# Optimization experiments

Hardware: AMD Instinct MI355X
Metric: run time of the kernel (lower is better)

The kernel has to match this reference:

```python
import jax, jax.numpy as jnp
import numpy as np

D_MODEL = 1024
NHEAD = 16
HEAD_DIM = D_MODEL // NHEAD
D_FF = 4096
BIAS_HID = 8
EPS = 1e-5


def _pair_bias(m, w1, b1, w2, b2):
    # m: [B,S,S] -> bias [B,S,S,nhead] via per-scalar MLP 1->hid->nhead
    h = jax.nn.relu(m[..., None] * w1 + b1)          # [B,S,S,hid]
    return jnp.einsum('bxyh,hn->bxyn', h, w2) + b2   # [B,S,S,nhead]


def _layernorm(x, g, b):
    mu = jnp.mean(x, axis=-1, keepdims=True)
    var = jnp.mean(jnp.square(x - mu), axis=-1, keepdims=True)
    return (x - mu) * jax.lax.rsqrt(var + EPS) * g + b


def setup_inputs() -> dict:
    key = jax.random.key(0)
    ks = jax.random.split(key, 20)
    B, S = 4, 1024
    sc = 1.0 / np.sqrt(D_MODEL)
    inp = {
        'src': jax.random.normal(ks[0], (B, S, D_MODEL), jnp.float32),
        't_deltas': jax.random.uniform(ks[1], (B, S, S), jnp.float32),
        'dists': jax.random.uniform(ks[2], (B, S, S), jnp.float32),
        'Wq': jax.random.normal(ks[3], (D_MODEL, D_MODEL), jnp.float32) * sc,
        'bq': jnp.zeros((D_MODEL,), jnp.float32),
        'Wk': jax.random.normal(ks[4], (D_MODEL, D_MODEL), jnp.float32) * sc,
        'bk': jnp.zeros((D_MODEL,), jnp.float32),
        'Wv': jax.random.normal(ks[5], (D_MODEL, D_MODEL), jnp.float32) * sc,
        'bv': jnp.zeros((D_MODEL,), jnp.float32),
        'tb_w1': jax.random.normal(ks[6], (BIAS_HID,), jnp.float32),
        'tb_b1': jnp.zeros((BIAS_HID,), jnp.float32),
        'tb_w2': jax.random.normal(ks[7], (BIAS_HID, NHEAD), jnp.float32) * 0.3,
        'tb_b2': jnp.zeros((NHEAD,), jnp.float32),
        'db_w1': jax.random.normal(ks[8], (BIAS_HID,), jnp.float32),
        'db_b1': jnp.zeros((BIAS_HID,), jnp.float32),
        'db_w2': jax.random.normal(ks[9], (BIAS_HID, NHEAD), jnp.float32) * 0.3,
        'db_b2': jnp.zeros((NHEAD,), jnp.float32),
        'W1': jax.random.normal(ks[10], (D_MODEL, D_FF), jnp.float32) * sc,
        'b1': jnp.zeros((D_FF,), jnp.float32),
        'W2': jax.random.normal(ks[11], (D_FF, D_MODEL), jnp.float32) / np.sqrt(D_FF),
        'b2': jnp.zeros((D_MODEL,), jnp.float32),
        'g1': jnp.ones((D_MODEL,), jnp.float32),
        'beta1': jnp.zeros((D_MODEL,), jnp.float32),
        'g2': jnp.ones((D_MODEL,), jnp.float32),
        'beta2': jnp.zeros((D_MODEL,), jnp.float32),
    }
    return inp


def reference(src, t_deltas, dists, Wq, bq, Wk, bk, Wv, bv,
              tb_w1, tb_b1, tb_w2, tb_b2, db_w1, db_b1, db_w2, db_b2,
              W1, b1, W2, b2, g1, beta1, g2, beta2):
    B, S, _ = src.shape
    # QKV projections -> [B, H, S, hd]
    q = (src @ Wq + bq).reshape(B, S, NHEAD, HEAD_DIM).transpose(0, 2, 1, 3)
    k = (src @ Wk + bk).reshape(B, S, NHEAD, HEAD_DIM).transpose(0, 2, 1, 3)
    v = (src @ Wv + bv).reshape(B, S, NHEAD, HEAD_DIM).transpose(0, 2, 1, 3)
    # scores scaled by sqrt(d_model) (as in the original, not head_dim)
    scores = jnp.einsum('bhqd,bhkd->bhqk', q, k) / jnp.sqrt(jnp.float32(D_MODEL))
    bias = (_pair_bias(t_deltas, tb_w1, tb_b1, tb_w2, tb_b2)
            + _pair_bias(dists, db_w1, db_b1, db_w2, db_b2))  # [B,S,S,H]
    scores = scores + bias.transpose(0, 3, 1, 2)
    attn = jax.nn.softmax(scores, axis=-1)
    out = jnp.einsum('bhqk,bhkd->bhqd', attn, v)
    out = out.transpose(0, 2, 1, 3).reshape(B, S, D_MODEL)
    x = _layernorm(src + out, g1, beta1)
    ffn = jax.nn.relu(x @ W1 + b1) @ W2 + b2
    return _layernorm(x + ffn, g2, beta2)
```

## Files before the change

kernel.cpp:

```cpp
#include <hip/hip_runtime.h>

typedef __bf16 bf16x8 __attribute__((ext_vector_type(8)));
typedef float f32x4 __attribute__((ext_vector_type(4)));
typedef unsigned short u16;

__device__ __forceinline__ u16 f2bf(float f) {
  union { float f; unsigned u; } x; x.f = f;
  unsigned r = x.u + 0x7fffu + ((x.u >> 16) & 1u);
  return (u16)(r >> 16);
}
__device__ __forceinline__ float bf2f(u16 u) {
  union { unsigned u; float f; } x; x.u = ((unsigned)u) << 16;
  return x.f;
}
__device__ __forceinline__ void gl_lds16(const void* g, void* l) {
  __builtin_amdgcn_global_load_lds(
      (const __attribute__((address_space(1))) void*)g,
      (__attribute__((address_space(3))) void*)l, 16, 0, 0);
}

__global__ __launch_bounds__(256) void cvt_kernel(const float* __restrict__ in,
                                                  u16* __restrict__ out, int n4) {
  int i = blockIdx.x * 256 + threadIdx.x;
  if (i >= n4) return;
  float4 v = ((const float4*)in)[i];
  unsigned lo = (unsigned)f2bf(v.x) | ((unsigned)f2bf(v.y) << 16);
  unsigned hi = (unsigned)f2bf(v.z) | ((unsigned)f2bf(v.w) << 16);
  uint2 u; u.x = lo; u.y = hi;
  *(uint2*)&out[(size_t)i * 4] = u;
}

__global__ __launch_bounds__(256) void tconv_kernel(const float* __restrict__ in,
                                                    u16* __restrict__ out, int R, int C) {
  __shared__ float tile[32][33];
  int c0 = blockIdx.x * 32, r0 = blockIdx.y * 32;
  int tx = threadIdx.x & 31, ty = threadIdx.x >> 5;
#pragma unroll
  for (int i = 0; i < 4; i++)
    tile[ty + i * 8][tx] = in[(size_t)(r0 + ty + i * 8) * C + c0 + tx];
  __syncthreads();
#pragma unroll
  for (int i = 0; i < 4; i++)
    out[(size_t)(c0 + ty + i * 8) * R + r0 + tx] = f2bf(tile[tx][ty + i * 8]);
}

__global__ __launch_bounds__(256) void bcat_kernel(const float* __restrict__ bq,
                                                   const float* __restrict__ bk,
                                                   const float* __restrict__ bv,
                                                   float* __restrict__ o) {
  int i = blockIdx.x * 256 + threadIdx.x;
  if (i >= 3072) return;
  o[i] = i < 1024 ? bq[i] : (i < 2048 ? bk[i - 1024] : bv[i - 2048]);
}

template <int EPI>
__global__ __launch_bounds__(512, 2) void gemm256_kernel(const u16* __restrict__ A,
                                                         const u16* __restrict__ Bt,
                                                         const float* __restrict__ bias,
                                                         void* __restrict__ out,
                                                         int M, int N, int K,
                                                         float qscale, int kslice) {
  __shared__ u16 lds[2][2][2][8192];
  int tid = threadIdx.x, w = tid >> 6, lane = tid & 63;
  int l16 = lane & 15, lhi = lane >> 4;
  int wr = w >> 2, wc = w & 3;
  int GX = gridDim.x;
  int nwg = GX * gridDim.y;
  int nlin = blockIdx.y * GX + blockIdx.x;
  int cpx = nwg >> 3;
  int sw = (nlin & 7) * cpx + (nlin >> 3);
  int m0 = (sw / GX) * 256, n0 = (sw % GX) * 256;
  int z = blockIdx.z;
  const u16* Ag = A + (size_t)m0 * K + z * kslice;
  const u16* Bg = Bt + (size_t)n0 * K + z * kslice;
  f32x4 acc[8][4] = {};
  int niter = kslice >> 7;

  int srow0 = tid >> 2;
  int sxor = ((tid & 3) ^ ((tid >> 3) & 3)) * 8;
  int rga = (lhi ^ ((l16 >> 1) & 3)) * 8;

  auto stage = [&](int buf, int op, int kh, const u16* Gt) {
#pragma unroll
    for (int ld = 0; ld < 2; ld++)
      gl_lds16(Gt + (size_t)(ld * 128 + srow0) * K + kh * 32 + sxor,
               &lds[buf][op][kh][ld * 4096 + w * 512]);
  };
  auto rdA = [&](int buf, int kh, int mq, bf16x8* af) {
#pragma unroll
    for (int j = 0; j < 4; j++)
      af[j] = *(const bf16x8*)&lds[buf][0][kh][(wr * 128 + mq * 64 + j * 16 + l16) * 32 + rga];
  };
  auto rdB = [&](int buf, int kh, bf16x8* bfr) {
#pragma unroll
    for (int nn = 0; nn < 4; nn++)
      bfr[nn] = *(const bf16x8*)&lds[buf][1][kh][(wc * 64 + nn * 16 + l16) * 32 + rga];
  };
  auto mma16 = [&](int mq, bf16x8* af, bf16x8* bfr) {
    __builtin_amdgcn_s_setprio(1);
#pragma unroll
    for (int j = 0; j < 4; j++)
#pragma unroll
      for (int nn = 0; nn < 4; nn++)
        acc[mq * 4 + j][nn] =
            __builtin_amdgcn_mfma_f32_16x16x32_bf16(af[j], bfr[nn], acc[mq * 4 + j][nn], 0, 0, 0);
    __builtin_amdgcn_s_setprio(0);
  };

#define PH_TAIL(MQ)                                          \
  __builtin_amdgcn_s_barrier();                              \
  asm volatile("s_waitcnt lgkmcnt(0)" ::: "memory");         \
  __builtin_amdgcn_sched_barrier(0);                         \
  mma16(MQ, af, bfr);                                        \
  __builtin_amdgcn_s_barrier();

  stage(0, 0, 0, Ag);       stage(0, 1, 0, Bg);
  stage(0, 0, 1, Ag);       stage(0, 1, 1, Bg);
  stage(1, 0, 0, Ag + 64);  stage(1, 1, 0, Bg + 64);
  asm volatile("s_waitcnt vmcnt(4)" ::: "memory");
  __builtin_amdgcn_s_barrier();

  for (int j = 0; j < niter; ++j) {
    const u16* A1 = Ag + (size_t)(2 * j + 1) * 64;
    const u16* B1 = Bg + (size_t)(2 * j + 1) * 64;
    const u16* A2 = Ag + (size_t)(2 * j + 2) * 64;
    const u16* B2 = Bg + (size_t)(2 * j + 2) * 64;
    bool more = (j + 1 < niter);
    bf16x8 af[4], bfr[4];
    rdA(0, 0, 0, af); rdB(0, 0, bfr);
    stage(1, 0, 1, A1);
    PH_TAIL(0)
    rdA(0, 0, 1, af);
    stage(1, 1, 1, B1);
    PH_TAIL(1)
    rdA(0, 1, 0, af); rdB(0, 1, bfr);
    if (more) stage(0, 0, 0, A2);
    PH_TAIL(0)
    rdA(0, 1, 1, af);
    if (more) {
      stage(0, 1, 0, B2);
      asm volatile("s_waitcnt vmcnt(4)" ::: "memory");
    } else {
      asm volatile("s_waitcnt vmcnt(0)" ::: "memory");
    }
    PH_TAIL(1)
    rdA(1, 0, 0, af); rdB(1, 0, bfr);
    if (more) stage(0, 0, 1, A2);
    PH_TAIL(0)
    rdA(1, 0, 1, af);
    if (more) stage(0, 1, 1, B2);
    PH_TAIL(1)
    rdA(1, 1, 0, af); rdB(1, 1, bfr);
    if (more) stage(1, 0, 0, A2 + 64);
    PH_TAIL(0)
    rdA(1, 1, 1, af);
    if (more) {
      stage(1, 1, 0, B2 + 64);
      asm volatile("s_waitcnt vmcnt(4)" ::: "memory");
    }
    PH_TAIL(1)
  }
#undef PH_TAIL

#pragma unroll
  for (int m = 0; m < 8; m++) {
    int gr = m0 + wr * 128 + (m >> 2) * 64 + (m & 3) * 16 + lhi * 4;
#pragma unroll
    for (int nn = 0; nn < 4; nn++) {
      int gc = n0 + wc * 64 + nn * 16 + l16;
      float bv;
      if (EPI == 0 || EPI == 3) bv = (z == 0 && bias) ? bias[gc] : 0.f;
      else bv = bias[gc];
      if (EPI == 2) {
        int seg = gc >> 10, c = gc & 1023, h = c >> 6, d = c & 63;
        float sc = (seg == 0) ? qscale : 1.f;
#pragma unroll
        for (int r = 0; r < 4; r++) {
          int row = gr + r;
          int b = row >> 10, s = row & 1023;
          size_t idx = ((((size_t)seg * 4 + b) * 16 + h) * 1024 + s) * 64 + d;
          ((u16*)out)[idx] = f2bf((acc[m][nn][r] + bv) * sc);
        }
      } else if (EPI == 1) {
#pragma unroll
        for (int r = 0; r < 4; r++)
          ((u16*)out)[(size_t)(gr + r) * N + gc] = f2bf(fmaxf(acc[m][nn][r] + bv, 0.f));
      } else if (EPI == 3) {
#pragma unroll
        for (int r = 0; r < 4; r++)
          ((u16*)out)[(size_t)z * M * N + (size_t)(gr + r) * N + gc] = f2bf(acc[m][nn][r] + bv);
      } else {
#pragma unroll
        for (int r = 0; r < 4; r++)
          ((float*)out)[(size_t)z * M * N + (size_t)(gr + r) * N + gc] = acc[m][nn][r] + bv;
      }
    }
  }
}

__global__ __launch_bounds__(256) void vtrans_kernel(const u16* __restrict__ v,
                                                     u16* __restrict__ vt) {
  __shared__ u16 t[64][72];
  int bh = blockIdx.y, s0 = blockIdx.x * 64;
  int tid = threadIdx.x;
  int r = tid >> 2, c = (tid & 3) * 16;
  const u16* src = v + ((size_t)bh * 1024 + s0 + r) * 64 + c;
  *(int4*)&t[r][c] = *(const int4*)src;
  *(int4*)&t[r][c + 8] = *(const int4*)(src + 8);
  __syncthreads();
  int d = tid >> 2, sc = (tid & 3) * 16;
  u16 tmp[16];
#pragma unroll
  for (int j = 0; j < 16; j++) tmp[j] = t[sc + j][d];
  u16* dst = vt + ((size_t)bh * 64 + d) * 1024 + s0 + sc;
  *(int4*)dst = *(int4*)&tmp[0];
  *(int4*)(dst + 8) = *(int4*)&tmp[8];
}

__global__ __launch_bounds__(256) void bias_kernel(
    const float* __restrict__ td, const float* __restrict__ dd,
    const float* __restrict__ tw1, const float* __restrict__ tb1,
    const float* __restrict__ tw2, const float* __restrict__ tb2,
    const float* __restrict__ dw1, const float* __restrict__ db1,
    const float* __restrict__ dw2, const float* __restrict__ db2,
    u16* __restrict__ biasout, int b0) {
  __shared__ float stw2[128], sdw2[128], sb2[16];
  __shared__ float stw1[8], stb1[8], sdw1[8], sdb1[8];
  int tid = threadIdx.x, x = blockIdx.x, bz = blockIdx.y;
  int b = b0 + bz;
  if (tid < 128) { stw2[tid] = tw2[tid]; sdw2[tid] = dw2[tid]; }
  if (tid < 16) sb2[tid] = tb2[tid] + db2[tid];
  if (tid < 8) { stw1[tid] = tw1[tid]; stb1[tid] = tb1[tid]; sdw1[tid] = dw1[tid]; sdb1[tid] = db1[tid]; }
  __syncthreads();
  float4 tv = ((const float4*)(td + ((size_t)b * 1024 + x) * 1024))[tid];
  float4 dv = ((const float4*)(dd + ((size_t)b * 1024 + x) * 1024))[tid];
  float tj[4] = {tv.x, tv.y, tv.z, tv.w};
  float dj[4] = {dv.x, dv.y, dv.z, dv.w};
  float ht[4][8], hd[4][8];
#pragma unroll
  for (int j = 0; j < 4; j++)
#pragma unroll
    for (int i = 0; i < 8; i++) {
      ht[j][i] = fmaxf(tj[j] * stw1[i] + stb1[i], 0.f);
      hd[j][i] = fmaxf(dj[j] * sdw1[i] + sdb1[i], 0.f);
    }
  u16* outb = biasout + (size_t)bz * 16 * 1024 * 1024 + (size_t)x * 1024 + tid * 4;
#pragma unroll
  for (int h = 0; h < 16; h++) {
    float a[4];
#pragma unroll
    for (int j = 0; j < 4; j++) {
      float s = sb2[h];
#pragma unroll
      for (int i = 0; i < 8; i++)
        s += ht[j][i] * stw2[i * 16 + h] + hd[j][i] * sdw2[i * 16 + h];
      a[j] = s;
    }
    unsigned lo = (unsigned)f2bf(a[0]) | ((unsigned)f2bf(a[1]) << 16);
    unsigned hi = (unsigned)f2bf(a[2]) | ((unsigned)f2bf(a[3]) << 16);
    uint2 u; u.x = lo; u.y = hi;
    *(uint2*)&outb[(size_t)h * 1024 * 1024] = u;
  }
}

#define LDA 72
__global__ __launch_bounds__(256) void attn_kernel(
    const u16* __restrict__ qg, const u16* __restrict__ kg, const u16* __restrict__ vtg,
    const u16* __restrict__ bias, float* __restrict__ attn_out, int b0) {
  __shared__ u16 Ks[64 * LDA];
  __shared__ u16 Vt[64 * LDA];
  __shared__ u16 Ps[64 * LDA];
  int tid = threadIdx.x;
  int w = tid >> 6, l = tid & 63, l16 = l & 15, lhi = l >> 4;
  int qt = blockIdx.x, h = blockIdx.y, bz = blockIdx.z;
  int b = b0 + bz;
  size_t bh = ((size_t)(b * 16 + h)) * 1024 * 64;
  const u16* biasb = bias + (size_t)bz * 16 * 1024 * 1024 + (size_t)h * 1024 * 1024;
  int qrow = qt * 64 + w * 16 + l16;
  bf16x8 qa[2];
  qa[0] = *(const bf16x8*)&qg[bh + (size_t)qrow * 64 + lhi * 8];
  qa[1] = *(const bf16x8*)&qg[bh + (size_t)qrow * 64 + 32 + lhi * 8];

  float m_run[4], l_run[4];
  f32x4 o[4] = {};
#pragma unroll
  for (int r = 0; r < 4; r++) { m_run[r] = -1e30f; l_run[r] = 0.f; }

  int kr0 = (tid * 2) >> 3, kc0 = ((tid * 2) & 7) * 8;
  int kr1 = (tid * 2 + 1) >> 3, kc1 = ((tid * 2 + 1) & 7) * 8;

  for (int kt = 0; kt < 16; kt++) {
    __syncthreads();
    *(int4*)&Ks[kr0 * LDA + kc0] = *(const int4*)&kg[bh + (size_t)(kt * 64 + kr0) * 64 + kc0];
    *(int4*)&Ks[kr1 * LDA + kc1] = *(const int4*)&kg[bh + (size_t)(kt * 64 + kr1) * 64 + kc1];
    *(int4*)&Vt[kr0 * LDA + kc0] = *(const int4*)&vtg[bh + (size_t)kr0 * 1024 + kt * 64 + kc0];
    *(int4*)&Vt[kr1 * LDA + kc1] = *(const int4*)&vtg[bh + (size_t)kr1 * 1024 + kt * 64 + kc1];
    __syncthreads();

    f32x4 s[4] = {};
    __builtin_amdgcn_s_setprio(1);
#pragma unroll
    for (int ni = 0; ni < 4; ni++)
#pragma unroll
      for (int ks = 0; ks < 2; ks++) {
        bf16x8 kb = *(const bf16x8*)&Ks[(ni * 16 + l16) * LDA + ks * 32 + lhi * 8];
        s[ni] = __builtin_amdgcn_mfma_f32_16x16x32_bf16(qa[ks], kb, s[ni], 0, 0, 0);
      }
    __builtin_amdgcn_s_setprio(0);
#pragma unroll
    for (int ni = 0; ni < 4; ni++)
#pragma unroll
      for (int r = 0; r < 4; r++) {
        int brow = qt * 64 + w * 16 + lhi * 4 + r;
        s[ni][r] += bf2f(biasb[(size_t)brow * 1024 + kt * 64 + ni * 16 + l16]);
      }
    float rs[4];
#pragma unroll
    for (int r = 0; r < 4; r++) {
      float m = fmaxf(fmaxf(s[0][r], s[1][r]), fmaxf(s[2][r], s[3][r]));
      m = fmaxf(m, __shfl_xor(m, 1, 16));
      m = fmaxf(m, __shfl_xor(m, 2, 16));
      m = fmaxf(m, __shfl_xor(m, 4, 16));
      m = fmaxf(m, __shfl_xor(m, 8, 16));
      float m2 = fmaxf(m_run[r], m);
      float sc = __expf(m_run[r] - m2);
      float sum = 0.f;
#pragma unroll
      for (int ni = 0; ni < 4; ni++) {
        float p = __expf(s[ni][r] - m2);
        s[ni][r] = p;
        sum += p;
      }
      sum += __shfl_xor(sum, 1, 16);
      sum += __shfl_xor(sum, 2, 16);
      sum += __shfl_xor(sum, 4, 16);
      sum += __shfl_xor(sum, 8, 16);
      l_run[r] = l_run[r] * sc + sum;
      m_run[r] = m2;
      rs[r] = sc;
    }
#pragma unroll
    for (int di = 0; di < 4; di++)
#pragma unroll
      for (int r = 0; r < 4; r++)
        o[di][r] *= rs[r];
#pragma unroll
    for (int ni = 0; ni < 4; ni++)
#pragma unroll
      for (int r = 0; r < 4; r++)
        Ps[(w * 16 + lhi * 4 + r) * LDA + ni * 16 + l16] = f2bf(s[ni][r]);
    __builtin_amdgcn_s_setprio(1);
#pragma unroll
    for (int ks = 0; ks < 2; ks++) {
      bf16x8 pa = *(const bf16x8*)&Ps[(w * 16 + l16) * LDA + ks * 32 + lhi * 8];
#pragma unroll
      for (int di = 0; di < 4; di++) {
        bf16x8 vb = *(const bf16x8*)&Vt[(di * 16 + l16) * LDA + ks * 32 + lhi * 8];
        o[di] = __builtin_amdgcn_mfma_f32_16x16x32_bf16(pa, vb, o[di], 0, 0, 0);
      }
    }
    __builtin_amdgcn_s_setprio(0);
  }
#pragma unroll
  for (int r = 0; r < 4; r++) {
    float inv = 1.f / l_run[r];
    int row = b * 1024 + qt * 64 + w * 16 + lhi * 4 + r;
#pragma unroll
    for (int di = 0; di < 4; di++)
      attn_out[(size_t)row * 1024 + h * 64 + di * 16 + l16] = o[di][r] * inv;
  }
}

__global__ __launch_bounds__(256) void ln_kernel(const float* __restrict__ a,
                                                 const float* __restrict__ r1,
                                                 const float* __restrict__ g,
                                                 const float* __restrict__ beta,
                                                 float* __restrict__ outf,
                                                 u16* __restrict__ outbf) {
  int row = blockIdx.x, tid = threadIdx.x;
  __shared__ float red[8];
  float4 va = ((const float4*)(a + (size_t)row * 1024))[tid];
  float4 vr = ((const float4*)(r1 + (size_t)row * 1024))[tid];
  float v[4] = {va.x + vr.x, va.y + vr.y, va.z + vr.z, va.w + vr.w};
  float s = v[0] + v[1] + v[2] + v[3];
#pragma unroll
  for (int off = 32; off >= 1; off >>= 1) s += __shfl_xor(s, off, 64);
  if ((tid & 63) == 0) red[tid >> 6] = s;
  __syncthreads();
  float mean = (red[0] + red[1] + red[2] + red[3]) * (1.f / 1024.f);
  float q = 0.f;
#pragma unroll
  for (int j = 0; j < 4; j++) { float d = v[j] - mean; q += d * d; }
#pragma unroll
  for (int off = 32; off >= 1; off >>= 1) q += __shfl_xor(q, off, 64);
  if ((tid & 63) == 0) red[4 + (tid >> 6)] = q;
  __syncthreads();
  float var = (red[4] + red[5] + red[6] + red[7]) * (1.f / 1024.f);
  float rstd = rsqrtf(var + 1e-5f);
  float4 gv = ((const float4*)g)[tid];
  float4 bv = ((const float4*)beta)[tid];
  float o0 = (v[0] - mean) * rstd * gv.x + bv.x;
  float o1 = (v[1] - mean) * rstd * gv.y + bv.y;
  float o2 = (v[2] - mean) * rstd * gv.z + bv.z;
  float o3 = (v[3] - mean) * rstd * gv.w + bv.w;
  float4 ov; ov.x = o0; ov.y = o1; ov.z = o2; ov.w = o3;
  ((float4*)(outf + (size_t)row * 1024))[tid] = ov;
  unsigned lo = (unsigned)f2bf(o0) | ((unsigned)f2bf(o1) << 16);
  unsigned hi = (unsigned)f2bf(o2) | ((unsigned)f2bf(o3) << 16);
  uint2 u; u.x = lo; u.y = hi;
  *(uint2*)&outbf[(size_t)row * 1024 + tid * 4] = u;
}

__global__ __launch_bounds__(256) void ln2_kernel(const float* __restrict__ x,
                                                  const u16* __restrict__ ff, int zs,
                                                  const float* __restrict__ g,
                                                  const float* __restrict__ beta,
                                                  float* __restrict__ out) {
  int row = blockIdx.x, tid = threadIdx.x;
  __shared__ float red[8];
  float4 xv = ((const float4*)(x + (size_t)row * 1024))[tid];
  float v[4] = {xv.x, xv.y, xv.z, xv.w};
  for (int z = 0; z < zs; z++) {
    uint2 u = *(const uint2*)&ff[(size_t)z * 4096 * 1024 + (size_t)row * 1024 + tid * 4];
    v[0] += bf2f(u.x & 0xffff); v[1] += bf2f(u.x >> 16);
    v[2] += bf2f(u.y & 0xffff); v[3] += bf2f(u.y >> 16);
  }
  float s = v[0] + v[1] + v[2] + v[3];
#pragma unroll
  for (int off = 32; off >= 1; off >>= 1) s += __shfl_xor(s, off, 64);
  if ((tid & 63) == 0) red[tid >> 6] = s;
  __syncthreads();
  float mean = (red[0] + red[1] + red[2] + red[3]) * (1.f / 1024.f);
  float q = 0.f;
#pragma unroll
  for (int j = 0; j < 4; j++) { float d = v[j] - mean; q += d * d; }
#pragma unroll
  for (int off = 32; off >= 1; off >>= 1) q += __shfl_xor(q, off, 64);
  if ((tid & 63) == 0) red[4 + (tid >> 6)] = q;
  __syncthreads();
  float var = (red[4] + red[5] + red[6] + red[7]) * (1.f / 1024.f);
  float rstd = rsqrtf(var + 1e-5f);
  float4 gv = ((const float4*)g)[tid];
  float4 bv = ((const float4*)beta)[tid];
  float4 ov;
  ov.x = (v[0] - mean) * rstd * gv.x + bv.x;
  ov.y = (v[1] - mean) * rstd * gv.y + bv.y;
  ov.z = (v[2] - mean) * rstd * gv.z + bv.z;
  ov.w = (v[3] - mean) * rstd * gv.w + bv.w;
  ((float4*)(out + (size_t)row * 1024))[tid] = ov;
}

extern "C" void kernel_launch(void* const* d_in, const int* in_sizes, int n_in,
                              void* d_out, int out_size, void* d_ws, size_t ws_size,
                              hipStream_t stream) {
  const float* src      = (const float*)d_in[0];
  const float* t_deltas = (const float*)d_in[1];
  const float* dists    = (const float*)d_in[2];
  const float* Wq = (const float*)d_in[3];
  const float* bq = (const float*)d_in[4];
  const float* Wk = (const float*)d_in[5];
  const float* bk = (const float*)d_in[6];
  const float* Wv = (const float*)d_in[7];
  const float* bv = (const float*)d_in[8];
  const float* tb_w1 = (const float*)d_in[9];
  const float* tb_b1 = (const float*)d_in[10];
  const float* tb_w2 = (const float*)d_in[11];
  const float* tb_b2 = (const float*)d_in[12];
  const float* db_w1 = (const float*)d_in[13];
  const float* db_b1 = (const float*)d_in[14];
  const float* db_w2 = (const float*)d_in[15];
  const float* db_b2 = (const float*)d_in[16];
  const float* W1 = (const float*)d_in[17];
  const float* b1 = (const float*)d_in[18];
  const float* W2 = (const float*)d_in[19];
  const float* b2 = (const float*)d_in[20];
  const float* g1 = (const float*)d_in[21];
  const float* beta1 = (const float*)d_in[22];
  const float* g2 = (const float*)d_in[23];
  const float* beta2 = (const float*)d_in[24];
  float* out = (float*)d_out;

  const size_t MB = 1024u * 1024;
  bool big = ws_size >= 150 * MB;
  int PB = big ? 2 : 1;
  int ZS = big ? 4 : 2;

  char* ws = (char*)d_ws;
  size_t off = 0;
  auto alloc = [&](size_t n) { void* p = ws + off; off += (n + 255) & ~(size_t)255; return p; };
  u16* src_bf  = (u16*)alloc(4096u * 1024 * 2);
  u16* wqkv_bt = (u16*)alloc(3072u * 1024 * 2);
  u16* w1_bt   = (u16*)alloc(4096u * 1024 * 2);
  u16* w2_bt   = (u16*)alloc(1024u * 4096 * 2);
  float* bcat  = (float*)alloc(3072u * 4);
  u16* qkv     = (u16*)alloc(3u * 4 * 16 * 1024 * 64 * 2);
  u16* vt      = (u16*)alloc(4u * 16 * 64 * 1024 * 2);
  u16* slab    = (u16*)alloc((size_t)PB * 16 * 1024 * 1024 * 2);
  float* attn_out = (float*)alloc(4096u * 1024 * 4);
  (void)in_sizes; (void)n_in; (void)out_size;

  u16* q_bf = qkv;
  u16* k_bf = qkv + 4u * 16 * 1024 * 64;
  u16* v_bf = qkv + 8u * 16 * 1024 * 64;
  float* x_f32 = (float*)qkv;
  u16*   x_bf  = (u16*)((char*)qkv + 16 * MB);
  u16*   h_bf  = (u16*)vt;
  u16*   ffnb  = big ? (u16*)((char*)slab + 24 * MB)
                     : (u16*)attn_out;

  cvt_kernel<<<4096, 256, 0, stream>>>(src, src_bf, 4096 * 1024 / 4);
  tconv_kernel<<<dim3(32, 32), 256, 0, stream>>>(Wq, wqkv_bt, 1024, 1024);
  tconv_kernel<<<dim3(32, 32), 256, 0, stream>>>(Wk, wqkv_bt + 1024u * 1024, 1024, 1024);
  tconv_kernel<<<dim3(32, 32), 256, 0, stream>>>(Wv, wqkv_bt + 2048u * 1024, 1024, 1024);
  tconv_kernel<<<dim3(128, 32), 256, 0, stream>>>(W1, w1_bt, 1024, 4096);
  tconv_kernel<<<dim3(32, 128), 256, 0, stream>>>(W2, w2_bt, 4096, 1024);
  bcat_kernel<<<12, 256, 0, stream>>>(bq, bk, bv, bcat);

  gemm256_kernel<2><<<dim3(12, 16, 1), 512, 0, stream>>>(src_bf, wqkv_bt, bcat, qkv,
                                                         4096, 3072, 1024, 1.f / 32.f, 1024);
  vtrans_kernel<<<dim3(16, 64), 256, 0, stream>>>(v_bf, vt);

  for (int p = 0; p < 4 / PB; p++) {
    bias_kernel<<<dim3(1024, PB), 256, 0, stream>>>(t_deltas, dists, tb_w1, tb_b1, tb_w2, tb_b2,
                                                    db_w1, db_b1, db_w2, db_b2, slab, p * PB);
    attn_kernel<<<dim3(16, 16, PB), 256, 0, stream>>>(q_bf, k_bf, vt, slab, attn_out, p * PB);
  }

  ln_kernel<<<4096, 256, 0, stream>>>(src, attn_out, g1, beta1, x_f32, x_bf);
  gemm256_kernel<1><<<dim3(16, 16, 1), 512, 0, stream>>>(x_bf, w1_bt, b1, h_bf,
                                                         4096, 4096, 1024, 1.f, 1024);
  gemm256_kernel<3><<<dim3(4, 16, ZS), 512, 0, stream>>>(h_bf, w2_bt, b2, ffnb,
                                                         4096, 1024, 4096, 1.f, 4096 / ZS);
  ln2_kernel<<<4096, 256, 0, stream>>>(x_f32, ffnb, ZS, g2, beta2, out);
}
```

Before: 297.0 us.

## Double-buffer GEMM LDS fragments and prefetch K/V/bias in attention

The GEMM main loop now double-buffers its register fragments (A0/A1, B0/B1), so LDS reads for the next phase are issued before the MFMAs of the current phase. It also drops the per-phase lgkmcnt(0) wait and retunes the vmcnt thresholds. Separately, the attention kernel prefetches the next K/V tile and the bias values into registers while computing the current tile, hiding global-load latency. This raises register pressure, and the hand-tuned waitcnt counts risk ordering errors if they are miscounted.

```diff
diff --git a/kernel.cpp b/kernel.cpp
--- a/kernel.cpp
+++ b/kernel.cpp
@@ -74,6 +74,7 @@
   const u16* Ag = A + (size_t)m0 * K + z * kslice;
   const u16* Bg = Bt + (size_t)n0 * K + z * kslice;
   f32x4 acc[8][4] = {};
+  bf16x8 A0[4], A1[4], B0[4], B1[4];
   int niter = kslice >> 7;
 
   int srow0 = tid >> 2;
@@ -86,81 +87,90 @@
       gl_lds16(Gt + (size_t)(ld * 128 + srow0) * K + kh * 32 + sxor,
                &lds[buf][op][kh][ld * 4096 + w * 512]);
   };
-  auto rdA = [&](int buf, int kh, int mq, bf16x8* af) {
-#pragma unroll
-    for (int j = 0; j < 4; j++)
-      af[j] = *(const bf16x8*)&lds[buf][0][kh][(wr * 128 + mq * 64 + j * 16 + l16) * 32 + rga];
+  auto rdA = [&](int buf, int kh, int mq, bf16x8 (&af)[4]) {
+#pragma unroll
+    for (int jf = 0; jf < 4; jf++)
+      af[jf] = *(const bf16x8*)&lds[buf][0][kh][(wr * 128 + mq * 64 + jf * 16 + l16) * 32 + rga];
   };
-  auto rdB = [&](int buf, int kh, bf16x8* bfr) {
+  auto rdB = [&](int buf, int kh, bf16x8 (&bfr)[4]) {
 #pragma unroll
     for (int nn = 0; nn < 4; nn++)
       bfr[nn] = *(const bf16x8*)&lds[buf][1][kh][(wc * 64 + nn * 16 + l16) * 32 + rga];
   };
-  auto mma16 = [&](int mq, bf16x8* af, bf16x8* bfr) {
+  auto mma16 = [&](int mq, bf16x8 (&af)[4], bf16x8 (&bfr)[4]) {
     __builtin_amdgcn_s_setprio(1);
 #pragma unroll
-    for (int j = 0; j < 4; j++)
+    for (int jf = 0; jf < 4; jf++)
 #pragma unroll
       for (int nn = 0; nn < 4; nn++)
-        acc[mq * 4 + j][nn] =
-            __builtin_amdgcn_mfma_f32_16x16x32_bf16(af[j], bfr[nn], acc[mq * 4 + j][nn], 0, 0, 0);
+        acc[mq * 4 + jf][nn] =
+            __builtin_amdgcn_mfma_f32_16x16x32_bf16(af[jf], bfr[nn], acc[mq * 4 + jf][nn], 0, 0, 0);
     __builtin_amdgcn_s_setprio(0);
   };
 
-#define PH_TAIL(MQ)                                          \
-  __builtin_amdgcn_s_barrier();                              \
-  asm volatile("s_waitcnt lgkmcnt(0)" ::: "memory");         \
-  __builtin_amdgcn_sched_barrier(0);                         \
-  mma16(MQ, af, bfr);                                        \
+  stage(0, 0, 0, Ag);      stage(0, 1, 0, Bg);
+  stage(0, 0, 1, Ag);      stage(0, 1, 1, Bg);
+  stage(1, 0, 0, Ag + 64); stage(1, 1, 0, Bg + 64);
+  asm volatile("s_waitcnt vmcnt(8)" ::: "memory");
   __builtin_amdgcn_s_barrier();
-
-  stage(0, 0, 0, Ag);       stage(0, 1, 0, Bg);
-  stage(0, 0, 1, Ag);       stage(0, 1, 1, Bg);
-  stage(1, 0, 0, Ag + 64);  stage(1, 1, 0, Bg + 64);
-  asm volatile("s_waitcnt vmcnt(4)" ::: "memory");
-  __builtin_amdgcn_s_barrier();
+  rdA(0, 0, 0, A1); rdB(0, 0, B0);
 
   for (int j = 0; j < niter; ++j) {
-    const u16* A1 = Ag + (size_t)(2 * j + 1) * 64;
-    const u16* B1 = Bg + (size_t)(2 * j + 1) * 64;
-    const u16* A2 = Ag + (size_t)(2 * j + 2) * 64;
-    const u16* B2 = Bg + (size_t)(2 * j + 2) * 64;
     bool more = (j + 1 < niter);
-    bf16x8 af[4], bfr[4];
-    rdA(0, 0, 0, af); rdB(0, 0, bfr);
-    stage(1, 0, 1, A1);
-    PH_TAIL(0)
-    rdA(0, 0, 1, af);
-    stage(1, 1, 1, B1);
-    PH_TAIL(1)
-    rdA(0, 1, 0, af); rdB(0, 1, bfr);
-    if (more) stage(0, 0, 0, A2);
-    PH_TAIL(0)
-    rdA(0, 1, 1, af);
-    if (more) {
-      stage(0, 1, 0, B2);
-      asm volatile("s_waitcnt vmcnt(4)" ::: "memory");
-    } else {
-      asm volatile("s_waitcnt vmcnt(0)" ::: "memory");
-    }
-    PH_TAIL(1)
-    rdA(1, 0, 0, af); rdB(1, 0, bfr);
-    if (more) stage(0, 0, 1, A2);
-    PH_TAIL(0)
-    rdA(1, 0, 1, af);
-    if (more) stage(0, 1, 1, B2);
-    PH_TAIL(1)
-    rdA(1, 1, 0, af); rdB(1, 1, bfr);
-    if (more) stage(1, 0, 0, A2 + 64);
-    PH_TAIL(0)
-    rdA(1, 1, 1, af);
-    if (more) {
-      stage(1, 1, 0, B2 + 64);
-      asm volatile("s_waitcnt vmcnt(4)" ::: "memory");
-    }
-    PH_TAIL(1)
-  }
-#undef PH_TAIL
+    const u16* At1 = Ag + (size_t)(2 * j + 1) * 64;
+    const u16* Bt1 = Bg + (size_t)(2 * j + 1) * 64;
+    const u16* At2 = Ag + (size_t)(2 * j + 2) * 64;
+    const u16* Bt2 = Bg + (size_t)(2 * j + 2) * 64;
+    const u16* At3 = Ag + (size_t)(2 * j + 3) * 64;
+    const u16* Bt3 = Bg + (size_t)(2 * j + 3) * 64;
+
+    __builtin_amdgcn_s_barrier();
+    rdA(0, 0, 1, A0);
+    stage(1, 0, 1, At1);
+    __builtin_amdgcn_sched_barrier(0);
+    mma16(0, A1, B0);
+    asm volatile("s_waitcnt vmcnt(6)" ::: "memory");
+    __builtin_amdgcn_s_barrier();
+    rdA(0, 1, 0, A1); rdB(0, 1, B1);
+    stage(1, 1, 1, Bt1);
+    __builtin_amdgcn_sched_barrier(0);
+    mma16(1, A0, B0);
+    __builtin_amdgcn_s_barrier();
+    rdA(0, 1, 1, A0);
+    if (more) stage(0, 0, 0, At2);
+    __builtin_amdgcn_sched_barrier(0);
+    mma16(0, A1, B1);
+    if (more) asm volatile("s_waitcnt vmcnt(6)" ::: "memory");
+    else      asm volatile("s_waitcnt vmcnt(4)" ::: "memory");
+    __builtin_amdgcn_s_barrier();
+    rdA(1, 0, 0, A1); rdB(1, 0, B0);
+    if (more) stage(0, 1, 0, Bt2);
+    __builtin_amdgcn_sched_barrier(0);
+    mma16(1, A0, B1);
+    __builtin_amdgcn_s_barrier();
+    rdA(1, 0, 1, A0);
+    if (more) stage(0, 0, 1, At2);
+    __builtin_amdgcn_sched_barrier(0);
+    mma16(0, A1, B0);
+    if (more) asm volatile("s_waitcnt vmcnt(6)" ::: "memory");
+    else      asm volatile("s_waitcnt vmcnt(0)" ::: "memory");
+    __builtin_amdgcn_s_barrier();
+    rdA(1, 1, 0, A1); rdB(1, 1, B1);
+    if (more) stage(0, 1, 1, Bt2);
+    __builtin_amdgcn_sched_barrier(0);
+    mma16(1, A0, B0);
+    __builtin_amdgcn_s_barrier();
+    rdA(1, 1, 1, A0);
+    if (more) stage(1, 0, 0, At3);
+    __builtin_amdgcn_sched_barrier(0);
+    mma16(0, A1, B1);
+    if (more) asm volatile("s_waitcnt vmcnt(6)" ::: "memory");
+    else      asm volatile("s_waitcnt vmcnt(0)" ::: "memory");
+    __builtin_amdgcn_s_barrier();
+    if (more) { rdA(0, 0, 0, A1); rdB(0, 0, B0); stage(1, 1, 0, Bt3); }
+    __builtin_amdgcn_sched_barrier(0);
+    mma16(1, A0, B1);
+  }
 
 #pragma unroll
   for (int m = 0; m < 8; m++) {
@@ -288,14 +298,40 @@
 
   int kr0 = (tid * 2) >> 3, kc0 = ((tid * 2) & 7) * 8;
   int kr1 = (tid * 2 + 1) >> 3, kc1 = ((tid * 2 + 1) & 7) * 8;
+  const u16* kbase = kg + bh;
+  const u16* vbase = vtg + bh;
+
+  int4 kA, kB, vA, vB;
+  u16 bpre[16];
+  auto issueKV = [&](int kt) {
+    kA = *(const int4*)&kbase[(size_t)(kt * 64 + kr0) * 64 + kc0];
+    kB = *(const int4*)&kbase[(size_t)(kt * 64 + kr1) * 64 + kc1];
+    vA = *(const int4*)&vbase[(size_t)kr0 * 1024 + kt * 64 + kc0];
+    vB = *(const int4*)&vbase[(size_t)kr1 * 1024 + kt * 64 + kc1];
+  };
+  auto issueBias = [&](int kt) {
+#pragma unroll
+    for (int ni = 0; ni < 4; ni++)
+#pragma unroll
+      for (int r = 0; r < 4; r++)
+        bpre[ni * 4 + r] =
+            biasb[(size_t)(qt * 64 + w * 16 + lhi * 4 + r) * 1024 + kt * 64 + ni * 16 + l16];
+  };
+  issueKV(0);
+  issueBias(0);
 
   for (int kt = 0; kt < 16; kt++) {
     __syncthreads();
-    *(int4*)&Ks[kr0 * LDA + kc0] = *(const int4*)&kg[bh + (size_t)(kt * 64 + kr0) * 64 + kc0];
-    *(int4*)&Ks[kr1 * LDA + kc1] = *(const int4*)&kg[bh + (size_t)(kt * 64 + kr1) * 64 + kc1];
-    *(int4*)&Vt[kr0 * LDA + kc0] = *(const int4*)&vtg[bh + (size_t)kr0 * 1024 + kt * 64 + kc0];
-    *(int4*)&Vt[kr1 * LDA + kc1] = *(const int4*)&vtg[bh + (size_t)kr1 * 1024 + kt * 64 + kc1];
+    *(int4*)&Ks[kr0 * LDA + kc0] = kA;
+    *(int4*)&Ks[kr1 * LDA + kc1] = kB;
+    *(int4*)&Vt[kr0 * LDA + kc0] = vA;
+    *(int4*)&Vt[kr1 * LDA + kc1] = vB;
     __syncthreads();
+    u16 bcur[16];
+#pragma unroll
+    for (int i = 0; i < 16; i++) bcur[i] = bpre[i];
+    if (kt + 1 < 16) { issueKV(kt + 1); issueBias(kt + 1); }
+    __builtin_amdgcn_sched_barrier(0);
 
     f32x4 s[4] = {};
     __builtin_amdgcn_s_setprio(1);
@@ -310,10 +346,8 @@
 #pragma unroll
     for (int ni = 0; ni < 4; ni++)
 #pragma unroll
-      for (int r = 0; r < 4; r++) {
-        int brow = qt * 64 + w * 16 + lhi * 4 + r;
-        s[ni][r] += bf2f(biasb[(size_t)brow * 1024 + kt * 64 + ni * 16 + l16]);
-      }
+      for (int r = 0; r < 4; r++)
+        s[ni][r] += bf2f(bcur[ni * 4 + r]);
     float rs[4];
 #pragma unroll
     for (int r = 0; r < 4; r++) {
```

Result: slower. 468.3 us (+57.7%).
